# Kernel tuning notes

Hardware: AMD Instinct MI355X
Metric: run time of the kernel (lower is better)

The kernel has to match this reference:

```python
import jax, jax.numpy as jnp
import numpy as np

B, C, H, W = 16, 768, 32, 32
HEADS = 12
EPS = 1e-5


def _make_rel_index(h, w):
    coords = np.stack(np.meshgrid(np.arange(h), np.arange(w), indexing='ij'))  # [2,h,w]
    cf = coords.reshape(2, -1)                      # [2,N]
    rel = cf[:, :, None] - cf[:, None, :]           # [2,N,N]
    rel = rel.transpose(1, 2, 0).copy()             # [N,N,2]
    rel[:, :, 0] += h - 1
    rel[:, :, 1] += w - 1
    rel[:, :, 0] *= 2 * w - 1
    return jnp.asarray(rel.sum(-1), dtype=jnp.int32)  # [N,N]


def setup_inputs() -> dict:
    key = jax.random.key(0)
    ks = jax.random.split(key, 8)
    s = 0.02
    return {
        'x': jax.random.normal(ks[0], (B, C, H, W), jnp.float32),
        'rpb_table': jax.random.normal(ks[1], ((2 * H - 1) * (2 * W - 1), HEADS), jnp.float32) * s,
        'g1': jnp.ones((C,), jnp.float32),
        'b1': jnp.zeros((C,), jnp.float32),
        'q_w': jax.random.normal(ks[2], (C, C), jnp.float32) * s,
        'q_b': jnp.zeros((C,), jnp.float32),
        'kv_w': jax.random.normal(ks[3], (2 * C, C), jnp.float32) * s,
        'kv_b': jnp.zeros((2 * C,), jnp.float32),
        'proj_w': jax.random.normal(ks[4], (C, C), jnp.float32) * s,
        'proj_b': jnp.zeros((C,), jnp.float32),
        'g2': jnp.ones((C,), jnp.float32),
        'b2': jnp.zeros((C,), jnp.float32),
        'fc1_w': jax.random.normal(ks[5], (4 * C, C), jnp.float32) * s,
        'fc1_b': jnp.zeros((4 * C,), jnp.float32),
        'fc2_w': jax.random.normal(ks[6], (C, 4 * C), jnp.float32) * s,
        'fc2_b': jnp.zeros((C,), jnp.float32),
        'rel_index': _make_rel_index(H, W),
    }


def _ln(t, g, b):
    m = t.mean(-1, keepdims=True)
    v = ((t - m) ** 2).mean(-1, keepdims=True)
    return (t - m) * jax.lax.rsqrt(v + EPS) * g + b


def reference(x, rpb_table, g1, b1, q_w, q_b, kv_w, kv_b, proj_w, proj_b,
              g2, b2, fc1_w, fc1_b, fc2_w, fc2_b, rel_index):
    b, c, h, w = x.shape
    n = h * w
    heads = rpb_table.shape[1]
    hd = c // heads
    scale = hd ** -0.5

    xt = x.reshape(b, c, n).transpose(0, 2, 1)  # [B,N,C]

    # --- attention branch ---
    xn = _ln(xt, g1, b1)
    q = (xn @ q_w.T + q_b).reshape(b, n, heads, hd).transpose(0, 2, 1, 3)  # [B,h,N,d]
    kv = (xn @ kv_w.T + kv_b).reshape(b, n, 2, heads, hd)
    k = kv[:, :, 0].transpose(0, 2, 1, 3)  # [B,h,N,d]
    v = kv[:, :, 1].transpose(0, 2, 1, 3)  # [B,h,N,d]
    attn = jnp.einsum('bhnd,bhmd->bhnm', q, k) * scale  # [B,h,N,N]
    bias = rpb_table[rel_index].transpose(2, 0, 1)      # [h,N,N]
    attn = jax.nn.softmax(attn + bias[None], axis=-1)
    o = jnp.einsum('bhnm,bhmd->bhnd', attn, v).transpose(0, 2, 1, 3).reshape(b, n, c)
    o = o @ proj_w.T + proj_b
    xt = xt + o

    # --- mlp branch ---
    xn = _ln(xt, g2, b2)
    h1 = jax.nn.gelu(xn @ fc1_w.T + fc1_b, approximate=False)
    xt = xt + (h1 @ fc2_w.T + fc2_b)

    return xt.transpose(0, 2, 1).reshape(b, c, h, w)
```

## Files before the change

kernel.cpp:

```cpp
#include <hip/hip_runtime.h>
#include <hip/hip_bf16.h>
#include <math.h>

typedef unsigned short u16;
typedef unsigned int u32;
typedef float f32x4 __attribute__((ext_vector_type(4)));
typedef short bf16x8 __attribute__((ext_vector_type(8)));
typedef unsigned short us4 __attribute__((ext_vector_type(4)));

struct alignas(16) F4 { float v[4]; };
template <int N> struct Tag { static constexpr int v = N; };

static constexpr int Bb = 16;
static constexpr int Cc = 768;
static constexpr int Nn = 1024;
static constexpr int NH = 12;
static constexpr int HD = 64;
static constexpr float LOG2E = 1.4426950408889634f;

static __device__ __forceinline__ u16 f2bf(float f) {
  union { float f; unsigned u; } v; v.f = f;
  unsigned u = v.u;
  u += 0x7fffu + ((u >> 16) & 1u);
  return (u16)(u >> 16);
}
static __device__ __forceinline__ float bf2f(u16 x) {
  union { unsigned u; float f; } v; v.u = ((unsigned)x) << 16; return v.f;
}
static __device__ __forceinline__ void gload16(const u16* g, u16* l) {
  __builtin_amdgcn_global_load_lds((const __attribute__((address_space(1))) u32*)g,
                                   (__attribute__((address_space(3))) u32*)l, 16, 0, 0);
}

__global__ __launch_bounds__(256) void k_pre_all(const float* __restrict__ q_w,
    const float* __restrict__ kv_w, const float* __restrict__ proj_w,
    const float* __restrict__ fc1_w, const float* __restrict__ fc2_w,
    const float* __restrict__ q_b, const float* __restrict__ kv_b,
    u16* __restrict__ wqkv, u16* __restrict__ wproj, u16* __restrict__ wfc1,
    u16* __restrict__ wfc2, float* __restrict__ bqkv,
    const float* __restrict__ x, float* __restrict__ xt,
    const float* __restrict__ rpb, const int* __restrict__ rel,
    u16* __restrict__ bias2) {
  const int bid = blockIdx.x, tid = threadIdx.x;
  if (bid < 27657) {
    int i = bid * 256 + tid;
    if (i < 589824)            wqkv[i] = f2bf(q_w[i]);
    else if (i < 1769472)      wqkv[i] = f2bf(kv_w[i - 589824]);
    else if (i < 2359296)      wproj[i - 1769472] = f2bf(proj_w[i - 1769472]);
    else if (i < 4718592)      wfc1[i - 2359296] = f2bf(fc1_w[i - 2359296]);
    else if (i < 7077888)      wfc2[i - 4718592] = f2bf(fc2_w[i - 4718592]);
    else if (i < 7078656)      bqkv[i - 7077888] = q_b[i - 7077888];
    else                       bqkv[i - 7077888] = kv_b[i - 7078656];
  } else if (bid < 39945) {
    __shared__ float tile[32][33];
    int j = bid - 27657;
    int n0 = (j & 31) * 32, c0 = ((j >> 5) % 24) * 32, b = j / 768;
    int tx = tid & 31, ty = tid >> 5;
    const float* xp = x + (size_t)b * Cc * Nn;
    #pragma unroll
    for (int i = 0; i < 32; i += 8)
      tile[ty + i][tx] = xp[(size_t)(c0 + ty + i) * Nn + n0 + tx];
    __syncthreads();
    float* xtp = xt + (size_t)b * Nn * Cc;
    #pragma unroll
    for (int i = 0; i < 32; i += 8)
      xtp[(size_t)(n0 + ty + i) * Cc + c0 + tx] = tile[tx][ty + i];
  } else {
    int idx = (bid - 39945) * 256 + tid;
    int k = idx & 1023, q = (idx >> 10) & 1023, h = idx >> 20;
    float v = rpb[rel[(size_t)q * Nn + k] * NH + h];
    bias2[((size_t)h * Nn + q) * Nn + k] = f2bf(v * LOG2E);
  }
}

__global__ __launch_bounds__(256) void k_layernorm(const float* __restrict__ in,
    const float* __restrict__ gam, const float* __restrict__ bet,
    u16* __restrict__ out) {
  int wave = threadIdx.x >> 6, lane = threadIdx.x & 63;
  int row = blockIdx.x * 4 + wave;
  const float* p = in + (size_t)row * Cc;
  float v[12]; float s = 0.f;
  #pragma unroll
  for (int i = 0; i < 12; i++) { v[i] = p[lane + i * 64]; s += v[i]; }
  #pragma unroll
  for (int m = 32; m >= 1; m >>= 1) s += __shfl_xor(s, m);
  float mean = s * (1.f / 768.f);
  float q = 0.f;
  #pragma unroll
  for (int i = 0; i < 12; i++) { float d = v[i] - mean; q += d * d; }
  #pragma unroll
  for (int m = 32; m >= 1; m >>= 1) q += __shfl_xor(q, m);
  float rstd = rsqrtf(q * (1.f / 768.f) + 1e-5f);
  u16* o = out + (size_t)row * Cc;
  #pragma unroll
  for (int i = 0; i < 12; i++) {
    int j = lane + i * 64;
    o[j] = f2bf((v[i] - mean) * rstd * gam[j] + bet[j]);
  }
}

struct GemmArgs {
  const u16* A; const u16* W; const float* bias;
  int M, N, K;
  const float* resIn;
  float* outF;
  u16* outBf;
  u16 *q, *k, *v;
};

template <int EPI>
__global__ __launch_bounds__(512, 2) void k_gemm(GemmArgs p) {
  extern __shared__ f32x4 smv[];
  u16* lA = (u16*)smv;
  u16* lB = (u16*)smv + 2 * 256 * 64;
  const int tid = threadIdx.x;
  const int wave = tid >> 6, lane = tid & 63;
  const int l15 = lane & 15, g = lane >> 4, h7 = l15 & 7;
  const int wr = wave >> 2, wc = wave & 3;
  const int rl = tid >> 3, cc8 = tid & 7;
  const int nwg = gridDim.x * gridDim.y;
  const int wg = blockIdx.y * gridDim.x + blockIdx.x;
  const int swz = (wg & 7) * (nwg >> 3) + (wg >> 3);
  const int bn = (swz % gridDim.x) * 256, bm = (swz / gridDim.x) * 256;
  const int K = p.K;

  f32x4 acc[8][4];
  #pragma unroll
  for (int i = 0; i < 8; i++)
    #pragma unroll
    for (int j = 0; j < 4; j++) acc[i][j] = (f32x4){0.f, 0.f, 0.f, 0.f};

  const u16* Ab = p.A + (size_t)bm * K;
  const u16* Wb = p.W + (size_t)bn * K;
  const int csw = (cc8 ^ (rl & 7)) * 8;

  auto stageA = [&](int buf, int k0, int half) {
    int r0 = half * 64 + rl, r1 = r0 + 128;
    gload16(Ab + (size_t)r0 * K + k0 + csw, &lA[buf * 16384 + r0 * 64 + cc8 * 8]);
    gload16(Ab + (size_t)r1 * K + k0 + csw, &lA[buf * 16384 + r1 * 64 + cc8 * 8]);
  };
  auto stageB = [&](int buf, int k0, int half) {
    int r0 = ((rl >> 5) << 6) + half * 32 + (rl & 31), r1 = r0 + 128;
    gload16(Wb + (size_t)r0 * K + k0 + csw, &lB[buf * 16384 + r0 * 64 + cc8 * 8]);
    gload16(Wb + (size_t)r1 * K + k0 + csw, &lB[buf * 16384 + r1 * 64 + cc8 * 8]);
  };

  bf16x8 a[4][2], bq[4][2];
  auto rdA = [&](int buf, int mt, int kk) {
    int row = wr * 128 + mt * 16 + l15;
    return *(const bf16x8*)&lA[buf * 16384 + row * 64 + (((kk << 2) + g) ^ h7) * 8];
  };
  auto rdB = [&](int buf, int nt, int kk) {
    int row = wc * 64 + nt * 16 + l15;
    return *(const bf16x8*)&lB[buf * 16384 + row * 64 + (((kk << 2) + g) ^ h7) * 8];
  };
  auto MF = [&](auto MBt, auto NBt) {
    constexpr int MB = decltype(MBt)::v, NB = decltype(NBt)::v;
    __builtin_amdgcn_s_setprio(1);
    #pragma unroll
    for (int kk = 0; kk < 2; kk++)
      #pragma unroll
      for (int mi = 0; mi < 4; mi++)
        #pragma unroll
        for (int ni = 0; ni < 2; ni++)
          acc[MB + mi][NB + ni] = __builtin_amdgcn_mfma_f32_16x16x32_bf16(
              a[mi][kk], bq[NB + ni][kk], acc[MB + mi][NB + ni], 0, 0, 0);
    __builtin_amdgcn_s_setprio(0);
  };

  stageA(0, 0, 0); stageB(0, 0, 0); stageB(0, 0, 1); stageA(0, 0, 1);
  stageA(1, 64, 0);
  asm volatile("s_waitcnt vmcnt(6)" ::: "memory");
  __builtin_amdgcn_s_barrier();

  auto TILE = [&](int t, auto tag) {
    constexpr int TAIL = decltype(tag)::v;
    const int buf = t & 1, nb = buf ^ 1;
    const int k1 = (t + 1) * 64;
    #pragma unroll
    for (int mi = 0; mi < 4; mi++) { a[mi][0] = rdA(buf, mi, 0); a[mi][1] = rdA(buf, mi, 1); }
    #pragma unroll
    for (int ni = 0; ni < 2; ni++) { bq[ni][0] = rdB(buf, ni, 0); bq[ni][1] = rdB(buf, ni, 1); }
    if constexpr (TAIL < 2) {
      stageB(nb, k1, 0);
      asm volatile("s_waitcnt vmcnt(6)" ::: "memory");
    } else {
      asm volatile("s_waitcnt vmcnt(2)" ::: "memory");
    }
    __builtin_amdgcn_s_barrier();
    __builtin_amdgcn_sched_barrier(0);
    MF(Tag<0>{}, Tag<0>{});
    #pragma unroll
    for (int ni = 0; ni < 2; ni++) { bq[2 + ni][0] = rdB(buf, 2 + ni, 0); bq[2 + ni][1] = rdB(buf, 2 + ni, 1); }
    if constexpr (TAIL < 2) {
      stageB(nb, k1, 1);
      asm volatile("s_waitcnt vmcnt(6)" ::: "memory");
    } else {
      asm volatile("s_waitcnt vmcnt(0)" ::: "memory");
    }
    __builtin_amdgcn_s_barrier();
    __builtin_amdgcn_sched_barrier(0);
    MF(Tag<0>{}, Tag<2>{});
    #pragma unroll
    for (int mi = 0; mi < 4; mi++) { a[mi][0] = rdA(buf, 4 + mi, 0); a[mi][1] = rdA(buf, 4 + mi, 1); }
    if constexpr (TAIL < 2) stageA(nb, k1, 1);
    __builtin_amdgcn_s_barrier();
    __builtin_amdgcn_sched_barrier(0);
    MF(Tag<4>{}, Tag<2>{});
    if constexpr (TAIL == 0) {
      stageA(buf, k1 + 64, 0);
      asm volatile("s_waitcnt vmcnt(6)" ::: "memory");
    } else if constexpr (TAIL == 1) {
      asm volatile("s_waitcnt vmcnt(4)" ::: "memory");
    }
    __builtin_amdgcn_s_barrier();
    __builtin_amdgcn_sched_barrier(0);
    MF(Tag<4>{}, Tag<0>{});
  };

  const int NT = K >> 6;
  for (int t = 0; t < NT - 2; ++t) TILE(t, Tag<0>{});
  TILE(NT - 2, Tag<1>{});
  TILE(NT - 1, Tag<2>{});

  #pragma unroll
  for (int mt = 0; mt < 8; mt++) {
    int rowb = bm + wr * 128 + mt * 16 + g * 4;
    #pragma unroll
    for (int nt = 0; nt < 4; nt++) {
      int col = bn + wc * 64 + nt * 16 + l15;
      float bias = p.bias[col];
      if constexpr (EPI == 0) {
        #pragma unroll
        for (int r = 0; r < 4; r++) {
          int grow = rowb + r;
          int bb = grow >> 10, nnq = grow & 1023;
          float val = acc[mt][nt][r] + bias;
          if (col < 768) {
            int head = col >> 6, d = col & 63;
            p.q[(((size_t)bb * NH + head) * Nn + nnq) * HD + d] = f2bf(val * (0.125f * LOG2E));
          } else {
            int j2 = col - 768;
            if (j2 < 768) {
              int head = j2 >> 6, d = j2 & 63;
              p.k[(((size_t)bb * NH + head) * Nn + nnq) * HD + d] = f2bf(val);
            } else {
              int j3 = j2 - 768;
              int head = j3 >> 6, d = j3 & 63;
              p.v[(((size_t)bb * NH + head) * HD + d) * Nn + nnq] = f2bf(val);
            }
          }
        }
      } else if constexpr (EPI == 1) {
        #pragma unroll
        for (int r = 0; r < 4; r++) {
          size_t idx = (size_t)(rowb + r) * p.N + col;
          p.outF[idx] = acc[mt][nt][r] + bias + p.resIn[idx];
        }
      } else if constexpr (EPI == 2) {
        #pragma unroll
        for (int r = 0; r < 4; r++) {
          float val = acc[mt][nt][r] + bias;
          val = 0.5f * val * (1.f + erff(val * 0.70710678118654752f));
          p.outBf[(size_t)(rowb + r) * p.N + col] = f2bf(val);
        }
      } else {
        int bb = rowb >> 10, n0 = rowb & 1023;
        F4 ov;
        #pragma unroll
        for (int r = 0; r < 4; r++)
          ov.v[r] = acc[mt][nt][r] + bias + p.resIn[(size_t)(rowb + r) * Cc + col];
        *(F4*)&p.outF[((size_t)bb * Cc + col) * Nn + n0] = ov;
      }
    }
  }
}

__global__ __launch_bounds__(512, 6) void k_attn(const u16* __restrict__ qt,
    const u16* __restrict__ kt_, const u16* __restrict__ vtt,
    const u16* __restrict__ bias2, u16* __restrict__ o) {
  __shared__ __align__(16) u16 lK[2][64 * 64];
  __shared__ __align__(16) u16 lV[2][64 * 64];
  __shared__ __align__(16) u16 lP[8][16 * 64];
  const int tid = threadIdx.x, wave = tid >> 6, lane = tid & 63;
  const int l15 = lane & 15, g = lane >> 4;
  const int i_ = blockIdx.x;
  const int slot = i_ >> 3;
  const int hx = (i_ & 7) * 12 + (slot >> 4);
  const int b = slot & 15, h = hx >> 3;
  const int q0 = (hx & 7) * 128 + wave * 16;
  const size_t bh  = ((size_t)b * NH + h) * Nn * HD;
  const size_t bhT = ((size_t)b * NH + h) * HD * Nn;
  const u16* biasH = bias2 + (size_t)h * Nn * Nn;
  u16* myP = &lP[wave][0];
  const float THR = 8.f * LOG2E;
  const int sRow = tid >> 3, sCol = tid & 7;
  const int h7 = l15 & 7;

  bf16x8 qa0, qa1;
  {
    const u16* qp = qt + bh + (size_t)(q0 + l15) * HD + g * 8;
    qa0 = *(const bf16x8*)qp;
    qa1 = *(const bf16x8*)(qp + 32);
  }
  bf16x8 ones;
  #pragma unroll
  for (int i = 0; i < 8; i++) ones[i] = (short)0x3F80;

  f32x4 ao[4];
  f32x4 al;
  float mr = -1e30f;
  #pragma unroll
  for (int d = 0; d < 4; d++) ao[d] = (f32x4){0.f, 0.f, 0.f, 0.f};
  al = (f32x4){0.f, 0.f, 0.f, 0.f};

  auto issueKV = [&](int kt0, int buf) {
    int cs = (sCol ^ (sRow & 7)) << 3;
    gload16(kt_ + bh + (size_t)(kt0 + sRow) * HD + cs, &lK[buf][sRow * 64 + sCol * 8]);
    gload16(vtt + bhT + (size_t)sRow * Nn + kt0 + cs, &lV[buf][sRow * 64 + sCol * 8]);
  };

  issueKV(0, 0);
  for (int t = 0; t < 16; ++t) {
    const int kt0 = t * 64, buf = t & 1;
    asm volatile("s_waitcnt vmcnt(0) lgkmcnt(0)" ::: "memory");
    __builtin_amdgcn_s_barrier();
    __builtin_amdgcn_sched_barrier(0);

    us4 bvv[4];
    #pragma unroll
    for (int nt = 0; nt < 4; nt++)
      bvv[nt] = *(const us4*)(biasH + (size_t)(q0 + l15) * Nn + kt0 + nt * 16 + g * 4);
    __builtin_amdgcn_sched_barrier(0);
    if (t < 15) issueKV(kt0 + 64, buf ^ 1);
    __builtin_amdgcn_sched_barrier(0);

    f32x4 s[4];
    __builtin_amdgcn_s_setprio(1);
    #pragma unroll
    for (int nt = 0; nt < 4; nt++) {
      const int row = nt * 16 + l15;
      bf16x8 kb0 = *(const bf16x8*)&lK[buf][row * 64 + ((g ^ h7) << 3)];
      bf16x8 kb1 = *(const bf16x8*)&lK[buf][row * 64 + (((g + 4) ^ h7) << 3)];
      s[nt] = __builtin_amdgcn_mfma_f32_16x16x32_bf16(kb0, qa0,
                (f32x4){0.f, 0.f, 0.f, 0.f}, 0, 0, 0);
      s[nt] = __builtin_amdgcn_mfma_f32_16x16x32_bf16(kb1, qa1, s[nt], 0, 0, 0);
    }
    __builtin_amdgcn_s_setprio(0);

    #pragma unroll
    for (int nt = 0; nt < 4; nt++) {
      #pragma unroll
      for (int r = 0; r < 4; r++) s[nt][r] += bf2f(bvv[nt][r]);
    }
    float pm = fmaxf(fmaxf(s[0][0], s[0][1]), fmaxf(s[0][2], s[0][3]));
    #pragma unroll
    for (int nt = 1; nt < 4; nt++)
      pm = fmaxf(pm, fmaxf(fmaxf(s[nt][0], s[nt][1]), fmaxf(s[nt][2], s[nt][3])));
    pm = fmaxf(pm, __shfl_xor(pm, 16));
    pm = fmaxf(pm, __shfl_xor(pm, 32));
    if (__any(pm > mr + THR)) {
      float mnew = fmaxf(mr, pm);
      float fac = __builtin_amdgcn_exp2f(mr - mnew);
      mr = mnew;
      f32x4 facO;
      #pragma unroll
      for (int r = 0; r < 4; r++) facO[r] = __shfl(fac, g * 4 + r);
      #pragma unroll
      for (int d = 0; d < 4; d++) ao[d] *= facO;
      al *= facO;
    }
    #pragma unroll
    for (int nt = 0; nt < 4; nt++) {
      #pragma unroll
      for (int r = 0; r < 4; r++)
        s[nt][r] = __builtin_amdgcn_exp2f(s[nt][r] - mr);
    }
    #pragma unroll
    for (int nt = 0; nt < 4; nt++) {
      u32 w0, w1;
      asm("v_cvt_pk_bf16_f32 %0, %1, %2" : "=v"(w0) : "v"(s[nt][0]), "v"(s[nt][1]));
      asm("v_cvt_pk_bf16_f32 %0, %1, %2" : "=v"(w1) : "v"(s[nt][2]), "v"(s[nt][3]));
      int cbase = (((2 * nt + (g >> 1)) ^ h7) << 3) + (g & 1) * 4;
      *(u32*)&myP[l15 * 64 + cbase]     = w0;
      *(u32*)&myP[l15 * 64 + cbase + 2] = w1;
    }
    __builtin_amdgcn_s_setprio(1);
    #pragma unroll
    for (int kc = 0; kc < 2; kc++) {
      bf16x8 pa = *(const bf16x8*)&myP[l15 * 64 + (((4 * kc + g) ^ h7) << 3)];
      al = __builtin_amdgcn_mfma_f32_16x16x32_bf16(pa, ones, al, 0, 0, 0);
      #pragma unroll
      for (int d = 0; d < 4; d++) {
        const int rv = d * 16 + l15;
        bf16x8 vb = *(const bf16x8*)&lV[buf][rv * 64 + (((kc * 4 + g) ^ h7) << 3)];
        ao[d] = __builtin_amdgcn_mfma_f32_16x16x32_bf16(pa, vb, ao[d], 0, 0, 0);
      }
    }
    __builtin_amdgcn_s_setprio(0);
  }
  f32x4 linv;
  #pragma unroll
  for (int r = 0; r < 4; r++) linv[r] = __builtin_amdgcn_rcpf(al[r]);
  #pragma unroll
  for (int r = 0; r < 4; r++) {
    int qg = q0 + g * 4 + r;
    u16* op = o + ((size_t)b * Nn + qg) * Cc + h * HD;
    #pragma unroll
    for (int d = 0; d < 4; d++)
      op[d * 16 + l15] = f2bf(ao[d][r] * linv[r]);
  }
}

extern "C" void kernel_launch(void* const* d_in, const int* in_sizes, int n_in,
                              void* d_out, int out_size, void* d_ws, size_t ws_size,
                              hipStream_t stream) {
  const float* x      = (const float*)d_in[0];
  const float* rpb    = (const float*)d_in[1];
  const float* g1     = (const float*)d_in[2];
  const float* b1v    = (const float*)d_in[3];
  const float* q_w    = (const float*)d_in[4];
  const float* q_b    = (const float*)d_in[5];
  const float* kv_w   = (const float*)d_in[6];
  const float* kv_b   = (const float*)d_in[7];
  const float* proj_w = (const float*)d_in[8];
  const float* proj_b = (const float*)d_in[9];
  const float* g2     = (const float*)d_in[10];
  const float* b2v    = (const float*)d_in[11];
  const float* fc1_w  = (const float*)d_in[12];
  const float* fc1_b  = (const float*)d_in[13];
  const float* fc2_w  = (const float*)d_in[14];
  const float* fc2_b  = (const float*)d_in[15];
  const int*   rel    = (const int*)d_in[16];
  float* out = (float*)d_out;

  char* ws = (char*)d_ws;
  size_t off = 0;
  auto alloc = [&](size_t bytes) -> void* {
    void* p = ws + off;
    off += (bytes + 255) & ~(size_t)255;
    return p;
  };
  u16*   wqkv  = (u16*)alloc((size_t)2304 * 768 * 2);
  u16*   wproj = (u16*)alloc((size_t)768 * 768 * 2);
  u16*   wfc1  = (u16*)alloc((size_t)3072 * 768 * 2);
  u16*   wfc2  = (u16*)alloc((size_t)768 * 3072 * 2);
  float* bqkv  = (float*)alloc((size_t)2304 * 4);
  float* xt    = (float*)alloc((size_t)16384 * 768 * 4);
  float* xt2   = (float*)alloc((size_t)16384 * 768 * 4);
  u16*   xn    = (u16*)alloc((size_t)16384 * 768 * 2);
  u16*   qb_   = (u16*)alloc((size_t)Bb * NH * Nn * HD * 2);
  u16*   kb_   = (u16*)alloc((size_t)Bb * NH * Nn * HD * 2);
  u16*   vb_   = (u16*)alloc((size_t)Bb * NH * Nn * HD * 2);
  u16*   ob_   = (u16*)alloc((size_t)16384 * 768 * 2);
  u16*   h1    = qb_;
  u16*   bias2 = (u16*)xt2;

  hipFuncSetAttribute((const void*)k_gemm<0>, hipFuncAttributeMaxDynamicSharedMemorySize, 131072);
  hipFuncSetAttribute((const void*)k_gemm<1>, hipFuncAttributeMaxDynamicSharedMemorySize, 131072);
  hipFuncSetAttribute((const void*)k_gemm<2>, hipFuncAttributeMaxDynamicSharedMemorySize, 131072);
  hipFuncSetAttribute((const void*)k_gemm<3>, hipFuncAttributeMaxDynamicSharedMemorySize, 131072);

  k_pre_all<<<89097, 256, 0, stream>>>(q_w, kv_w, proj_w, fc1_w, fc2_w, q_b, kv_b,
                                       wqkv, wproj, wfc1, wfc2, bqkv,
                                       x, xt, rpb, rel, bias2);

  k_layernorm<<<4096, 256, 0, stream>>>(xt, g1, b1v, xn);

  GemmArgs ga = {};
  ga.A = xn; ga.W = wqkv; ga.bias = bqkv; ga.M = 16384; ga.N = 2304; ga.K = 768;
  ga.q = qb_; ga.k = kb_; ga.v = vb_;
  k_gemm<0><<<dim3(9, 64), 512, 131072, stream>>>(ga);

  k_attn<<<1536, 512, 0, stream>>>(qb_, kb_, vb_, bias2, ob_);

  GemmArgs gp = {};
  gp.A = ob_; gp.W = wproj; gp.bias = proj_b; gp.M = 16384; gp.N = 768; gp.K = 768;
  gp.resIn = xt; gp.outF = xt2;
  k_gemm<1><<<dim3(3, 64), 512, 131072, stream>>>(gp);

  k_layernorm<<<4096, 256, 0, stream>>>(xt2, g2, b2v, xn);

  GemmArgs gf1 = {};
  gf1.A = xn; gf1.W = wfc1; gf1.bias = fc1_b; gf1.M = 16384; gf1.N = 3072; gf1.K = 768;
  gf1.outBf = h1;
  k_gemm<2><<<dim3(12, 64), 512, 131072, stream>>>(gf1);

  GemmArgs gf2 = {};
  gf2.A = h1; gf2.W = wfc2; gf2.bias = fc2_b; gf2.M = 16384; gf2.N = 768; gf2.K = 3072;
  gf2.resIn = xt2; gf2.outF = out;
  k_gemm<3><<<dim3(3, 64), 512, 131072, stream>>>(gf2);
}
```

Before: 546.5 us.

## Process 128 keys per iteration in attention kernel with larger K/V tiles

```diff
diff --git a/kernel.cpp b/kernel.cpp
--- a/kernel.cpp
+++ b/kernel.cpp
@@ -276,11 +276,11 @@
   }
 }
 
-__global__ __launch_bounds__(512, 6) void k_attn(const u16* __restrict__ qt,
+__global__ __launch_bounds__(512, 4) void k_attn(const u16* __restrict__ qt,
     const u16* __restrict__ kt_, const u16* __restrict__ vtt,
     const u16* __restrict__ bias2, u16* __restrict__ o) {
-  __shared__ __align__(16) u16 lK[2][64 * 64];
-  __shared__ __align__(16) u16 lV[2][64 * 64];
+  __shared__ __align__(16) u16 lK[2][128 * 64];
+  __shared__ __align__(16) u16 lV[2][2][64 * 64];
   __shared__ __align__(16) u16 lP[8][16 * 64];
   const int tid = threadIdx.x, wave = tid >> 6, lane = tid & 63;
   const int l15 = lane & 15, g = lane >> 4;
@@ -314,31 +314,37 @@
   for (int d = 0; d < 4; d++) ao[d] = (f32x4){0.f, 0.f, 0.f, 0.f};
   al = (f32x4){0.f, 0.f, 0.f, 0.f};
 
-  auto issueKV = [&](int kt0, int buf) {
+  auto issueKV = [&](int kt0, int bufi) {
     int cs = (sCol ^ (sRow & 7)) << 3;
-    gload16(kt_ + bh + (size_t)(kt0 + sRow) * HD + cs, &lK[buf][sRow * 64 + sCol * 8]);
-    gload16(vtt + bhT + (size_t)sRow * Nn + kt0 + cs, &lV[buf][sRow * 64 + sCol * 8]);
+    gload16(kt_ + bh + (size_t)(kt0 + sRow) * HD + cs,
+            &lK[bufi][sRow * 64 + sCol * 8]);
+    gload16(kt_ + bh + (size_t)(kt0 + 64 + sRow) * HD + cs,
+            &lK[bufi][(64 + sRow) * 64 + sCol * 8]);
+    gload16(vtt + bhT + (size_t)sRow * Nn + kt0 + cs,
+            &lV[bufi][0][sRow * 64 + sCol * 8]);
+    gload16(vtt + bhT + (size_t)sRow * Nn + kt0 + 64 + cs,
+            &lV[bufi][1][sRow * 64 + sCol * 8]);
   };
 
   issueKV(0, 0);
-  for (int t = 0; t < 16; ++t) {
-    const int kt0 = t * 64, buf = t & 1;
+  for (int t = 0; t < 8; ++t) {
+    const int kt0 = t * 128, buf = t & 1;
     asm volatile("s_waitcnt vmcnt(0) lgkmcnt(0)" ::: "memory");
     __builtin_amdgcn_s_barrier();
     __builtin_amdgcn_sched_barrier(0);
 
-    us4 bvv[4];
-    #pragma unroll
-    for (int nt = 0; nt < 4; nt++)
+    us4 bvv[8];
+    #pragma unroll
+    for (int nt = 0; nt < 8; nt++)
       bvv[nt] = *(const us4*)(biasH + (size_t)(q0 + l15) * Nn + kt0 + nt * 16 + g * 4);
     __builtin_amdgcn_sched_barrier(0);
-    if (t < 15) issueKV(kt0 + 64, buf ^ 1);
-    __builtin_amdgcn_sched_barrier(0);
-
-    f32x4 s[4];
+    if (t < 7) issueKV(kt0 + 128, buf ^ 1);
+    __builtin_amdgcn_sched_barrier(0);
+
+    f32x4 s[8];
     __builtin_amdgcn_s_setprio(1);
     #pragma unroll
-    for (int nt = 0; nt < 4; nt++) {
+    for (int nt = 0; nt < 8; nt++) {
       const int row = nt * 16 + l15;
       bf16x8 kb0 = *(const bf16x8*)&lK[buf][row * 64 + ((g ^ h7) << 3)];
       bf16x8 kb1 = *(const bf16x8*)&lK[buf][row * 64 + (((g + 4) ^ h7) << 3)];
@@ -349,13 +355,13 @@
     __builtin_amdgcn_s_setprio(0);
 
     #pragma unroll
-    for (int nt = 0; nt < 4; nt++) {
+    for (int nt = 0; nt < 8; nt++) {
       #pragma unroll
       for (int r = 0; r < 4; r++) s[nt][r] += bf2f(bvv[nt][r]);
     }
     float pm = fmaxf(fmaxf(s[0][0], s[0][1]), fmaxf(s[0][2], s[0][3]));
     #pragma unroll
-    for (int nt = 1; nt < 4; nt++)
+    for (int nt = 1; nt < 8; nt++)
       pm = fmaxf(pm, fmaxf(fmaxf(s[nt][0], s[nt][1]), fmaxf(s[nt][2], s[nt][3])));
     pm = fmaxf(pm, __shfl_xor(pm, 16));
     pm = fmaxf(pm, __shfl_xor(pm, 32));
@@ -371,7 +377,7 @@
       al *= facO;
     }
     #pragma unroll
-    for (int nt = 0; nt < 4; nt++) {
+    for (int nt = 0; nt < 8; nt++) {
       #pragma unroll
       for (int r = 0; r < 4; r++)
         s[nt][r] = __builtin_amdgcn_exp2f(s[nt][r] - mr);
@@ -393,7 +399,30 @@
       #pragma unroll
       for (int d = 0; d < 4; d++) {
         const int rv = d * 16 + l15;
-        bf16x8 vb = *(const bf16x8*)&lV[buf][rv * 64 + (((kc * 4 + g) ^ h7) << 3)];
+        bf16x8 vb = *(const bf16x8*)&lV[buf][0][rv * 64 + (((kc * 4 + g) ^ h7) << 3)];
+        ao[d] = __builtin_amdgcn_mfma_f32_16x16x32_bf16(pa, vb, ao[d], 0, 0, 0);
+      }
+    }
+    __builtin_amdgcn_s_setprio(0);
+    #pragma unroll
+    for (int nt = 4; nt < 8; nt++) {
+      const int ntl = nt - 4;
+      u32 w0, w1;
+      asm("v_cvt_pk_bf16_f32 %0, %1, %2" : "=v"(w0) : "v"(s[nt][0]), "v"(s[nt][1]));
+      asm("v_cvt_pk_bf16_f32 %0, %1, %2" : "=v"(w1) : "v"(s[nt][2]), "v"(s[nt][3]));
+      int cbase = (((2 * ntl + (g >> 1)) ^ h7) << 3) + (g & 1) * 4;
+      *(u32*)&myP[l15 * 64 + cbase]     = w0;
+      *(u32*)&myP[l15 * 64 + cbase + 2] = w1;
+    }
+    __builtin_amdgcn_s_setprio(1);
+    #pragma unroll
+    for (int kc = 0; kc < 2; kc++) {
+      bf16x8 pa = *(const bf16x8*)&myP[l15 * 64 + (((4 * kc + g) ^ h7) << 3)];
+      al = __builtin_amdgcn_mfma_f32_16x16x32_bf16(pa, ones, al, 0, 0, 0);
+      #pragma unroll
+      for (int d = 0; d < 4; d++) {
+        const int rv = d * 16 + l15;
+        bf16x8 vb = *(const bf16x8*)&lV[buf][1][rv * 64 + (((kc * 4 + g) ^ h7) << 3)];
         ao[d] = __builtin_amdgcn_mfma_f32_16x16x32_bf16(pa, vb, ao[d], 0, 0, 0);
       }
     }
```

After: 540.5 us. Within noise of the previous version (-1.1%).
